# Kernel optimization log

Measured on AMD Instinct MI355X. Metric: run time of the kernel, lower is better.

The kernel has to match this reference:

```python
import jax, jax.numpy as jnp
import numpy as np

B, S, D = 2, 2048, 2048
H, HK, HD = 16, 4, 128          # query heads, kv heads, head dim (H*HD == D)
HID = 4 * D                      # SwiGLU hidden (mult=4)
WIN, SINK = 1024, 4              # sliding window, attention sink tokens
EPS = 1e-6
ROPE_BASE = 10000.0


def rmsnorm(x, g):
    return x * jax.lax.rsqrt(jnp.mean(x * x, axis=-1, keepdims=True) + EPS) * g


def rope_tables(seq_len, head_dim):
    inv = 1.0 / (ROPE_BASE ** (jnp.arange(0, head_dim, 2, dtype=jnp.float32) / head_dim))
    ang = jnp.arange(seq_len, dtype=jnp.float32)[:, None] * inv[None, :]  # [S, HD/2]
    return jnp.cos(ang), jnp.sin(ang)


def apply_rope(x, cos, sin):
    # x: [B, S, h, HD]; rotate-half convention
    x1, x2 = jnp.split(x, 2, axis=-1)
    c = cos[None, :, None, :]
    s = sin[None, :, None, :]
    return jnp.concatenate([x1 * c - x2 * s, x2 * c + x1 * s], axis=-1)


def setup_inputs() -> dict:
    key = jax.random.key(0)
    ks = jax.random.split(key, 10)
    p = 0.02
    return {
        "x": jax.random.normal(ks[0], (B, S, D), dtype=jnp.float32),
        "g1": jnp.ones((D,), dtype=jnp.float32),
        "g2": jnp.ones((D,), dtype=jnp.float32),
        "wq": jax.random.normal(ks[1], (D, H * HD), dtype=jnp.float32) * p,
        "wk": jax.random.normal(ks[2], (D, HK * HD), dtype=jnp.float32) * p,
        "wv": jax.random.normal(ks[3], (D, HK * HD), dtype=jnp.float32) * p,
        "wo": jax.random.normal(ks[4], (H * HD, D), dtype=jnp.float32) * p,
        "w_gate": jax.random.normal(ks[5], (D, HID), dtype=jnp.float32) * p,
        "w_up": jax.random.normal(ks[6], (D, HID), dtype=jnp.float32) * p,
        "w_down": jax.random.normal(ks[7], (HID, D), dtype=jnp.float32) * p,
    }


def reference(x, g1, g2, wq, wk, wv, wo, w_gate, w_up, w_down):
    # ---- pre-norm attention ----
    h = rmsnorm(x, g1)
    q = (h @ wq).reshape(B, S, H, HD)
    k = (h @ wk).reshape(B, S, HK, HD)
    v = (h @ wv).reshape(B, S, HK, HD)

    cos, sin = rope_tables(S, HD)
    q = apply_rope(q, cos, sin)
    k = apply_rope(k, cos, sin)

    # GQA: expand kv heads to query heads
    rep = H // HK
    k = jnp.repeat(k, rep, axis=2)  # [B, S, H, HD]
    v = jnp.repeat(v, rep, axis=2)

    scores = jnp.einsum("bqhd,bkhd->bhqk", q, k) / jnp.sqrt(jnp.float32(HD))

    # causal + sliding-window + attention-sink mask
    i = jnp.arange(S)[:, None]
    j = jnp.arange(S)[None, :]
    allowed = (j <= i) & (((i - j) < WIN) | (j < SINK))  # [S, S]
    scores = jnp.where(allowed[None, None], scores, jnp.float32(-1e9))

    attn = jax.nn.softmax(scores, axis=-1)
    a = jnp.einsum("bhqk,bkhd->bqhd", attn, v).reshape(B, S, H * HD) @ wo

    x = x + a

    # ---- pre-norm SwiGLU FFN ----
    h2 = rmsnorm(x, g2)
    ffn = (jax.nn.silu(h2 @ w_gate) * (h2 @ w_up)) @ w_down
    return x + ffn
```

## Files before the change

### kernel.cpp

```cpp
#include <hip/hip_runtime.h>
#include <hip/hip_bf16.h>
#include <stdint.h>

#define TOK 4096
#define SEQ 2048
#define DM 2048
#define NH 16
#define NKV 4
#define HDIM 128
#define HID 8192
#define WIN 1024
#define SINKN 4

typedef float f32x4 __attribute__((ext_vector_type(4)));
typedef __bf16 bf16x8 __attribute__((ext_vector_type(8)));
typedef unsigned short u16;
typedef unsigned int u32;

#define VM(n) asm volatile("s_waitcnt vmcnt(" #n ")" ::: "memory")
#define LG(n) asm volatile("s_waitcnt lgkmcnt(" #n ")" ::: "memory")
#define SCHED0 __builtin_amdgcn_sched_barrier(0)

__device__ __forceinline__ u16 f2bf(float f) {
  union { float f; u32 u; } v; v.f = f;
  return (u16)((v.u + 0x7fffu + ((v.u >> 16) & 1u)) >> 16);
}
__device__ __forceinline__ float bf2f(u16 h) {
  union { u32 u; float f; } v; v.u = ((u32)h) << 16;
  return v.f;
}
__device__ __forceinline__ f32x4 mfma16(bf16x8 a, bf16x8 b, f32x4 c) {
  return __builtin_amdgcn_mfma_f32_16x16x32_bf16(a, b, c, 0, 0, 0);
}
__device__ __forceinline__ void gld16(const u16* g, u16* l) {
  __builtin_amdgcn_global_load_lds(
      (const __attribute__((address_space(1))) u32*)g,
      (__attribute__((address_space(3))) u32*)l, 16, 0, 0);
}
__device__ __forceinline__ void bar() {
  asm volatile("s_barrier" ::: "memory");
}
__device__ __forceinline__ void swz_rc(int c, int& row, int& k8) {
  row = 2 * (c >> 3) + (((c >> 2) & 1) ^ ((c >> 4) & 1));
  k8 = (c & 3) ^ (row & 3);
}
__device__ __forceinline__ void raster8(int wg, int nwg, int nbx, int& bx, int& by) {
  int cpx = nwg >> 3;
  int s = (wg & 7) * cpx + (wg >> 3);
  by = 8 * (s / (8 * nbx)) + (s & 7);
  bx = (s >> 3) % nbx;
}

__global__ __launch_bounds__(256)
void wtrans(const float* __restrict__ in, u16* __restrict__ out, int K, int N)
{
  __shared__ float t[32][33];
  int tx = threadIdx.x & 31, ty = threadIdx.x >> 5;
  int bx = blockIdx.x, by = blockIdx.y;
  #pragma unroll
  for (int i = 0; i < 4; i++) {
    int r = ty + i * 8;
    t[r][tx] = in[(size_t)(by * 32 + r) * N + bx * 32 + tx];
  }
  __syncthreads();
  #pragma unroll
  for (int i = 0; i < 4; i++) {
    int r = ty + i * 8;
    out[(size_t)(bx * 32 + r) * K + by * 32 + tx] = f2bf(t[tx][r]);
  }
}

__global__ __launch_bounds__(256)
void vtrans(const u16* __restrict__ in, int ld, u16* __restrict__ out)
{
  __shared__ u16 t[32][33];
  int tx = threadIdx.x & 31, ty = threadIdx.x >> 5;
  int bx = blockIdx.x;
  int by = blockIdx.y;
  #pragma unroll
  for (int i = 0; i < 4; i++) {
    int r = ty + i * 8;
    t[r][tx] = in[(size_t)(by * 32 + r) * ld + bx * 32 + tx];
  }
  __syncthreads();
  int b = (by * 32) >> 11;
  int s0 = (by * 32) & (SEQ - 1);
  #pragma unroll
  for (int i = 0; i < 4; i++) {
    int c = bx * 32 + ty + i * 8;
    out[(size_t)(b * (NKV * HDIM) + c) * SEQ + s0 + tx] = t[tx][ty + i * 8];
  }
}

__global__ __launch_bounds__(256)
void rope_table_k(float* __restrict__ ct, float* __restrict__ st)
{
  int idx = blockIdx.x * 256 + threadIdx.x;
  int pos = idx >> 6, d = idx & 63;
  float inv = powf(10000.0f, -(float)d / 64.0f);
  float a = (float)pos * inv;
  ct[idx] = cosf(a);
  st[idx] = sinf(a);
}

__global__ void rope_apply_k(u16* __restrict__ q, int ld,
                             const float* __restrict__ ct,
                             const float* __restrict__ st, float scale)
{
  int t = blockIdx.x;
  int hh = threadIdx.x >> 6;
  int d = threadIdx.x & 63;
  int pos = t & (SEQ - 1);
  size_t base = (size_t)t * ld + hh * HDIM + d;
  float x1 = bf2f(q[base]), x2 = bf2f(q[base + 64]);
  float c = ct[pos * 64 + d], s = st[pos * 64 + d];
  q[base]      = f2bf((x1 * c - x2 * s) * scale);
  q[base + 64] = f2bf((x2 * c + x1 * s) * scale);
}

__global__ __launch_bounds__(256)
void rmsnorm_k(const float* __restrict__ x, const float* __restrict__ g,
               u16* __restrict__ o)
{
  int row = blockIdx.x;
  int tid = threadIdx.x;
  const float* xr = x + (size_t)row * DM;
  float4 v0 = *(const float4*)(xr + tid * 8);
  float4 v1 = *(const float4*)(xr + tid * 8 + 4);
  float ss = v0.x*v0.x + v0.y*v0.y + v0.z*v0.z + v0.w*v0.w
           + v1.x*v1.x + v1.y*v1.y + v1.z*v1.z + v1.w*v1.w;
  #pragma unroll
  for (int d = 1; d < 64; d <<= 1) ss += __shfl_xor(ss, d);
  __shared__ float red[4];
  if ((tid & 63) == 0) red[tid >> 6] = ss;
  __syncthreads();
  float inv = rsqrtf((red[0] + red[1] + red[2] + red[3]) * (1.0f / DM) + 1e-6f);
  float4 g0 = *(const float4*)(g + tid * 8);
  float4 g1 = *(const float4*)(g + tid * 8 + 4);
  ushort4 o0, o1;
  o0.x = f2bf(v0.x * inv * g0.x); o0.y = f2bf(v0.y * inv * g0.y);
  o0.z = f2bf(v0.z * inv * g0.z); o0.w = f2bf(v0.w * inv * g0.w);
  o1.x = f2bf(v1.x * inv * g1.x); o1.y = f2bf(v1.y * inv * g1.y);
  o1.z = f2bf(v1.z * inv * g1.z); o1.w = f2bf(v1.w * inv * g1.w);
  *(ushort4*)(o + (size_t)row * DM + tid * 8) = o0;
  *(ushort4*)(o + (size_t)row * DM + tid * 8 + 4) = o1;
}

template<int EPI>
__global__ __launch_bounds__(512, 1)
void gemmp(const u16* __restrict__ A, const u16* __restrict__ Bt,
           u16* __restrict__ Cb, float* __restrict__ Cf,
           const float* __restrict__ X, int M, int N, int K, int nbx)
{
  constexpr int ASZ = 128 * 64;
  constexpr int SLOT = ASZ + 256 * 64;
  __shared__ u16 lds[3 * SLOT];

  int bx, by;
  raster8(blockIdx.x, gridDim.x, nbx, bx, by);
  int m0 = by * 128;
  int n0 = bx * 256;

  int tid = threadIdx.x;
  int l = tid & 63, w = tid >> 6;
  int l16 = l & 15, lg = l >> 4;
  int wr = w >> 2, wc = w & 3;

  int aoff[4][2], boff[4][2];
  #pragma unroll
  for (int m = 0; m < 4; m++)
    #pragma unroll
    for (int kk = 0; kk < 2; kk++) {
      int row = wr * 64 + m * 16 + l16;
      aoff[m][kk] = ((row * 128 + kk * 64 + lg * 16) ^ ((row & 7) << 4)) >> 1;
    }
  #pragma unroll
  for (int n = 0; n < 4; n++)
    #pragma unroll
    for (int kk = 0; kk < 2; kk++) {
      int br = wc * 64 + n * 16 + l16;
      boff[n][kk] = ASZ + (((br * 128 + kk * 64 + lg * 16) ^ ((br & 7) << 4)) >> 1);
    }

  int urow = tid >> 3;
  int cc = (tid & 7) ^ (urow & 7);
  const u16* pA[2];
  const u16* pB[4];
  pA[0] = A + (size_t)(m0 + urow) * K + cc * 8;
  pA[1] = A + (size_t)(m0 + 64 + urow) * K + cc * 8;
  #pragma unroll
  for (int u = 0; u < 4; u++)
    pB[u] = Bt + (size_t)(n0 + u * 64 + urow) * K + cc * 8;

  const int NT = K >> 6;

  auto stA = [&](int tt, int u) {
    gld16(pA[u] + (size_t)tt * 64, lds + (tt % 3) * SLOT + u * 4096 + tid * 8);
  };
  auto stB = [&](int tt, int u) {
    gld16(pB[u] + (size_t)tt * 64, lds + (tt % 3) * SLOT + ASZ + u * 4096 + tid * 8);
  };

  #pragma unroll
  for (int u = 0; u < 4; u++) stB(0, u);
  stA(0, 0); stA(0, 1);
  #pragma unroll
  for (int u = 0; u < 4; u++) stB(1, u);
  stA(1, 0); stA(1, 1);
  VM(6);
  bar();

  f32x4 acc[4][4];
  f32x4 zero = {0.f, 0.f, 0.f, 0.f};
  #pragma unroll
  for (int m = 0; m < 4; m++)
    #pragma unroll
    for (int n = 0; n < 4; n++) acc[m][n] = zero;

  for (int t = 0; t < NT; ++t) {
    u16* cur = lds + (t % 3) * SLOT;
    const bool st = (t + 2 < NT);

    if (st) { stB(t + 2, 0); stB(t + 2, 1); stB(t + 2, 2); }
    bf16x8 a[4][2], b[2][2], c2[2][2];
    #pragma unroll
    for (int m = 0; m < 4; m++) {
      a[m][0] = *(const bf16x8*)(cur + aoff[m][0]);
      a[m][1] = *(const bf16x8*)(cur + aoff[m][1]);
    }
    #pragma unroll
    for (int n = 0; n < 2; n++) {
      b[n][0] = *(const bf16x8*)(cur + boff[n][0]);
      b[n][1] = *(const bf16x8*)(cur + boff[n][1]);
    }
    SCHED0;
    #pragma unroll
    for (int n = 0; n < 2; n++) {
      c2[n][0] = *(const bf16x8*)(cur + boff[n + 2][0]);
      c2[n][1] = *(const bf16x8*)(cur + boff[n + 2][1]);
    }
    bar();
    LG(4);
    SCHED0;
    __builtin_amdgcn_s_setprio(1);
    #pragma unroll
    for (int m = 0; m < 4; m++)
      #pragma unroll
      for (int n = 0; n < 2; n++) {
        acc[m][n] = mfma16(a[m][0], b[n][0], acc[m][n]);
        acc[m][n] = mfma16(a[m][1], b[n][1], acc[m][n]);
      }
    __builtin_amdgcn_s_setprio(0);
    SCHED0;
    bar();

    if (st) { stB(t + 2, 3); stA(t + 2, 0); stA(t + 2, 1); }
    if (st) { VM(6); }
    else if (t + 1 < NT) { VM(0); }
    bar();
    LG(0);
    SCHED0;
    __builtin_amdgcn_s_setprio(1);
    #pragma unroll
    for (int m = 0; m < 4; m++)
      #pragma unroll
      for (int n = 0; n < 2; n++) {
        acc[m][n + 2] = mfma16(a[m][0], c2[n][0], acc[m][n + 2]);
        acc[m][n + 2] = mfma16(a[m][1], c2[n][1], acc[m][n + 2]);
      }
    __builtin_amdgcn_s_setprio(0);
    SCHED0;
    bar();
  }

  #pragma unroll
  for (int m = 0; m < 4; m++) {
    int row = m0 + wr * 64 + m * 16 + lg * 4;
    #pragma unroll
    for (int n = 0; n < 4; n++) {
      int col = n0 + wc * 64 + n * 16 + l16;
      #pragma unroll
      for (int r = 0; r < 4; r++) {
        size_t idx = (size_t)(row + r) * N + col;
        float v = acc[m][n][r];
        if (EPI == 0) {
          Cb[idx] = f2bf(v);
        } else if (EPI == 1) {
          Cf[idx] = X[idx] + v;
        } else {
          Cf[idx] += v;
        }
      }
    }
  }
}

__global__ __launch_bounds__(512, 1)
void gemm256gu(const u16* __restrict__ A, const u16* __restrict__ Bg,
               const u16* __restrict__ Bu, u16* __restrict__ Gu,
               int K, int nbx)
{
  constexpr int SLOT = 32768;
  __shared__ u16 lds[2 * SLOT];

  int bx, by;
  raster8(blockIdx.x, gridDim.x, nbx, bx, by);
  int m0 = by * 256, n0 = bx * 128;

  int tid = threadIdx.x;
  int l = tid & 63, w = tid >> 6;
  int l16 = l & 15, lg = l >> 4;
  int wr = w >> 2, wc = w & 3;

  int sw = (l16 & 7) << 4;
  int aoffk[2], boffk[2];
  #pragma unroll
  for (int kk = 0; kk < 2; kk++) {
    aoffk[kk] = ((wr * 128 + l16) * 128 + ((kk * 64 + lg * 16) ^ sw)) >> 1;
    boffk[kk] = 16384 + ((((wc * 32 + l16) * 128) + ((kk * 64 + lg * 16) ^ sw)) >> 1);
  }

  int rh = tid >> 3;
  int cc = (tid & 7) ^ (rh & 7);
  const u16* pA0[2]; const u16* pA1[2]; const u16* pBg[2]; const u16* pBu[2];
  #pragma unroll
  for (int ll = 0; ll < 2; ll++) {
    pA0[ll] = A + (size_t)(m0 + ll * 64 + rh) * K + cc * 8;
    pA1[ll] = A + (size_t)(m0 + 128 + ll * 64 + rh) * K + cc * 8;
    pBg[ll] = Bg + (size_t)(n0 + ll * 64 + rh) * K + cc * 8;
    pBu[ll] = Bu + (size_t)(n0 + ll * 64 + rh) * K + cc * 8;
  }

  const int NT = K >> 6;

  auto stA0 = [&](int tt) {
    u16* d = lds + (tt & 1) * SLOT;
    gld16(pA0[0] + (size_t)tt * 64, d + tid * 8);
    gld16(pA0[1] + (size_t)tt * 64, d + 4096 + tid * 8);
  };
  auto stA1 = [&](int tt) {
    u16* d = lds + (tt & 1) * SLOT + 8192;
    gld16(pA1[0] + (size_t)tt * 64, d + tid * 8);
    gld16(pA1[1] + (size_t)tt * 64, d + 4096 + tid * 8);
  };
  auto stBg = [&](int tt) {
    u16* d = lds + (tt & 1) * SLOT + 16384;
    gld16(pBg[0] + (size_t)tt * 64, d + tid * 8);
    gld16(pBg[1] + (size_t)tt * 64, d + 4096 + tid * 8);
  };
  auto stBu = [&](int tt) {
    u16* d = lds + (tt & 1) * SLOT + 16384 + 8192;
    gld16(pBu[0] + (size_t)tt * 64, d + tid * 8);
    gld16(pBu[1] + (size_t)tt * 64, d + 4096 + tid * 8);
  };

  stA0(0); stA1(0); stBg(0); stBu(0);
  stA0(1); stBg(1); stBu(1);
  VM(6);
  bar();

  f32x4 acc[8][4];
  f32x4 zero = {0.f, 0.f, 0.f, 0.f};
  #pragma unroll
  for (int m = 0; m < 8; m++)
    #pragma unroll
    for (int n = 0; n < 4; n++) acc[m][n] = zero;

  for (int t = 0; t < NT; ++t) {
    u16* cur = lds + (t & 1) * SLOT;

    if (t + 1 < NT) stA1(t + 1);
    bf16x8 a0[4], a1[4], b0[4];
    #pragma unroll
    for (int m = 0; m < 4; m++)
      a0[m] = *(const bf16x8*)(cur + aoffk[0] + m * 1024);
    #pragma unroll
    for (int n = 0; n < 4; n++)
      b0[n] = *(const bf16x8*)(cur + boffk[0] + (n & 1) * 1024 + (n >> 1) * 8192);
    SCHED0;
    #pragma unroll
    for (int m = 0; m < 4; m++)
      a1[m] = *(const bf16x8*)(cur + aoffk[0] + 4096 + m * 1024);
    bar();
    LG(4);
    SCHED0;
    __builtin_amdgcn_s_setprio(1);
    #pragma unroll
    for (int m = 0; m < 4; m++)
      #pragma unroll
      for (int n = 0; n < 4; n++)
        acc[m][n] = mfma16(a0[m], b0[n], acc[m][n]);
    __builtin_amdgcn_s_setprio(0);
    SCHED0;
    bar();

    bf16x8 a2[4], b1[4];
    #pragma unroll
    for (int m = 0; m < 4; m++)
      a2[m] = *(const bf16x8*)(cur + aoffk[1] + m * 1024);
    #pragma unroll
    for (int n = 0; n < 4; n++)
      b1[n] = *(const bf16x8*)(cur + boffk[1] + (n & 1) * 1024 + (n >> 1) * 8192);
    bar();
    LG(8);
    SCHED0;
    __builtin_amdgcn_s_setprio(1);
    #pragma unroll
    for (int m = 0; m < 4; m++)
      #pragma unroll
      for (int n = 0; n < 4; n++)
        acc[4 + m][n] = mfma16(a1[m], b0[n], acc[4 + m][n]);
    __builtin_amdgcn_s_setprio(0);
    SCHED0;
    bar();

    bf16x8 a3[4];
    #pragma unroll
    for (int m = 0; m < 4; m++)
      a3[m] = *(const bf16x8*)(cur + aoffk[1] + 4096 + m * 1024);
    bar();
    LG(4);
    SCHED0;
    __builtin_amdgcn_s_setprio(1);
    #pragma unroll
    for (int m = 0; m < 4; m++)
      #pragma unroll
      for (int n = 0; n < 4; n++)
        acc[m][n] = mfma16(a2[m], b1[n], acc[m][n]);
    __builtin_amdgcn_s_setprio(0);
    SCHED0;
    bar();

    if (t + 2 < NT) { stA0(t + 2); stBg(t + 2); stBu(t + 2); }
    bar();
    LG(0);
    SCHED0;
    __builtin_amdgcn_s_setprio(1);
    #pragma unroll
    for (int m = 0; m < 4; m++)
      #pragma unroll
      for (int n = 0; n < 4; n++)
        acc[4 + m][n] = mfma16(a3[m], b1[n], acc[4 + m][n]);
    __builtin_amdgcn_s_setprio(0);
    SCHED0;
    if (t + 2 < NT) { VM(6); }
    else if (t + 1 < NT) { VM(0); }
    bar();
  }

  #pragma unroll
  for (int m = 0; m < 8; m++) {
    int row = m0 + wr * 128 + m * 16 + lg * 4;
    #pragma unroll
    for (int n = 0; n < 2; n++) {
      int col = n0 + wc * 32 + n * 16 + l16;
      #pragma unroll
      for (int r = 0; r < 4; r++) {
        float gt = acc[m][n][r];
        float up = acc[m][n + 2][r];
        float sg = gt / (1.0f + __expf(-gt));
        Gu[(size_t)(row + r) * HID + col] = f2bf(sg * up);
      }
    }
  }
}

__global__ __launch_bounds__(256)
void attn_k(const u16* __restrict__ qb, int ldq,
            const u16* __restrict__ kb, int ldk,
            const u16* __restrict__ vbt, u16* __restrict__ ao)
{
  int q0 = blockIdx.x * 128;
  int h = blockIdx.y;
  int b = blockIdx.z;
  int hk = h >> 2;
  int tid = threadIdx.x;
  int w = tid >> 6, l = tid & 63;
  int l16 = l & 15, lg = l >> 4;

  __shared__ u16 Ks[32 * 128];
  __shared__ u16 Vt[128 * 32];
  __shared__ u16 Ps[4][32 * 40];
  u16* Pw = Ps[w];

  bf16x8 qf[2][4];
  #pragma unroll
  for (int m = 0; m < 2; m++)
    #pragma unroll
    for (int kd = 0; kd < 4; kd++) {
      int row = q0 + w * 32 + m * 16 + l16;
      qf[m][kd] = *(const bf16x8*)(qb + (size_t)(b * SEQ + row) * ldq
                                   + h * HDIM + kd * 32 + lg * 8);
    }

  f32x4 oacc[2][8];
  float mrun[2][4], lrun[2][4];
  f32x4 zero = {0.f, 0.f, 0.f, 0.f};
  #pragma unroll
  for (int m = 0; m < 2; m++) {
    #pragma unroll
    for (int nd = 0; nd < 8; nd++) oacc[m][nd] = zero;
    #pragma unroll
    for (int r = 0; r < 4; r++) { mrun[m][r] = -1e9f; lrun[m][r] = 0.f; }
  }

  int kr0 = tid >> 4,        kc0 = (tid & 15) ^ (kr0 & 7);
  int kr1 = (tid + 256) >> 4, kc1 = (tid & 15) ^ (kr1 & 7);
  int vd0, vk0, vd1, vk1;
  swz_rc(tid, vd0, vk0);
  swz_rc(tid + 256, vd1, vk1);
  const u16* kbase = kb + (size_t)(b * SEQ) * ldk + hk * HDIM;
  const u16* vbase = vbt + (size_t)(b * NKV + hk) * HDIM * SEQ;

  int koff[2][4];
  #pragma unroll
  for (int n = 0; n < 2; n++)
    #pragma unroll
    for (int kd = 0; kd < 4; kd++) {
      int key = n * 16 + l16;
      koff[n][kd] = ((key * 128) + kd * 32 + lg * 8) ^ ((key & 7) * 8);
    }
  int voff[8];
  #pragma unroll
  for (int nd = 0; nd < 8; nd++) {
    int d = nd * 16 + l16;
    voff[nd] = (d * 32 + lg * 8) ^ ((d & 7) * 8);
  }

  int lo = (q0 >= WIN) ? ((q0 - (WIN - 1)) >> 5) : 0;
  int hi = (q0 + 127) >> 5;

  for (int it = (lo > 0 ? lo - 1 : 0); it <= hi; ++it) {
    int kt = (it < lo) ? 0 : it;
    gld16(kbase + (size_t)(kt * 32 + kr0) * ldk + kc0 * 8, Ks + tid * 8);
    gld16(kbase + (size_t)(kt * 32 + kr1) * ldk + kc1 * 8, Ks + (tid + 256) * 8);
    gld16(vbase + (size_t)vd0 * SEQ + kt * 32 + vk0 * 8, Vt + tid * 8);
    gld16(vbase + (size_t)vd1 * SEQ + kt * 32 + vk1 * 8, Vt + (tid + 256) * 8);
    __syncthreads();

    f32x4 sacc[2][2];
    sacc[0][0] = zero; sacc[0][1] = zero; sacc[1][0] = zero; sacc[1][1] = zero;
    #pragma unroll
    for (int kd = 0; kd < 4; kd++) {
      bf16x8 kf0 = *(const bf16x8*)(Ks + koff[0][kd]);
      bf16x8 kf1 = *(const bf16x8*)(Ks + koff[1][kd]);
      #pragma unroll
      for (int m = 0; m < 2; m++) {
        sacc[m][0] = mfma16(qf[m][kd], kf0, sacc[m][0]);
        sacc[m][1] = mfma16(qf[m][kd], kf1, sacc[m][1]);
      }
    }

    #pragma unroll
    for (int m = 0; m < 2; m++) {
      float sc[4];
      #pragma unroll
      for (int r = 0; r < 4; r++) {
        int i = q0 + w * 32 + m * 16 + lg * 4 + r;
        int j0 = kt * 32 + l16;
        int j1 = j0 + 16;
        float s0 = sacc[m][0][r];
        float s1 = sacc[m][1][r];
        bool ok0 = (j0 <= i) && ((i - j0 < WIN) || (j0 < SINKN));
        bool ok1 = (j1 <= i) && ((i - j1 < WIN) || (j1 < SINKN));
        s0 = ok0 ? s0 : -1e9f;
        s1 = ok1 ? s1 : -1e9f;
        float mx = fmaxf(s0, s1);
        mx = fmaxf(mx, __shfl_xor(mx, 1));
        mx = fmaxf(mx, __shfl_xor(mx, 2));
        mx = fmaxf(mx, __shfl_xor(mx, 4));
        mx = fmaxf(mx, __shfl_xor(mx, 8));
        float mold = mrun[m][r];
        float mnew = fmaxf(mold, mx);
        float scl = __expf(mold - mnew);
        mrun[m][r] = mnew;
        float p0 = __expf(s0 - mnew);
        float p1 = __expf(s1 - mnew);
        int prow = m * 16 + lg * 4 + r;
        Pw[prow * 40 + l16] = f2bf(p0);
        Pw[prow * 40 + 16 + l16] = f2bf(p1);
        float ps = p0 + p1;
        ps += __shfl_xor(ps, 1);
        ps += __shfl_xor(ps, 2);
        ps += __shfl_xor(ps, 4);
        ps += __shfl_xor(ps, 8);
        lrun[m][r] = lrun[m][r] * scl + ps;
        sc[r] = scl;
      }
      #pragma unroll
      for (int nd = 0; nd < 8; nd++) {
        oacc[m][nd][0] *= sc[0];
        oacc[m][nd][1] *= sc[1];
        oacc[m][nd][2] *= sc[2];
        oacc[m][nd][3] *= sc[3];
      }
    }

    bf16x8 pa0 = *(const bf16x8*)(Pw + l16 * 40 + lg * 8);
    bf16x8 pa1 = *(const bf16x8*)(Pw + (16 + l16) * 40 + lg * 8);
    #pragma unroll
    for (int nd = 0; nd < 8; nd++) {
      bf16x8 vf = *(const bf16x8*)(Vt + voff[nd]);
      oacc[0][nd] = mfma16(pa0, vf, oacc[0][nd]);
      oacc[1][nd] = mfma16(pa1, vf, oacc[1][nd]);
    }
    __syncthreads();
  }

  #pragma unroll
  for (int m = 0; m < 2; m++)
    #pragma unroll
    for (int r = 0; r < 4; r++) {
      float invl = 1.0f / lrun[m][r];
      int row = q0 + w * 32 + m * 16 + lg * 4 + r;
      #pragma unroll
      for (int nd = 0; nd < 8; nd++) {
        int col = nd * 16 + l16;
        ao[(size_t)(b * SEQ + row) * (NH * HDIM) + h * HDIM + col] =
            f2bf(oacc[m][nd][r] * invl);
      }
    }
}

extern "C" void kernel_launch(void* const* d_in, const int* in_sizes, int n_in,
                              void* d_out, int out_size, void* d_ws, size_t ws_size,
                              hipStream_t stream)
{
  (void)in_sizes; (void)n_in; (void)out_size;
  const float* x  = (const float*)d_in[0];
  const float* g1 = (const float*)d_in[1];
  const float* g2 = (const float*)d_in[2];
  const float* wq = (const float*)d_in[3];
  const float* wk = (const float*)d_in[4];
  const float* wv = (const float*)d_in[5];
  const float* wo = (const float*)d_in[6];
  const float* wg = (const float*)d_in[7];
  const float* wu = (const float*)d_in[8];
  const float* wd = (const float*)d_in[9];
  float* out = (float*)d_out;

  char* ws = (char*)d_ws;
  size_t off = 0;
  auto alloc = [&](size_t bytes) {
    char* p = ws + off;
    off += (bytes + 255) & ~(size_t)255;
    return p;
  };
  const int NQKV = 3072;
  u16* wqkv_t = (u16*)alloc((size_t)NQKV * DM * 2);
  u16* wo_t   = (u16*)alloc((size_t)DM * DM * 2);
  u16* wg_t   = (u16*)alloc((size_t)HID * DM * 2);
  u16* wu_t   = (u16*)alloc((size_t)HID * DM * 2);
  u16* wd_t   = (u16*)alloc((size_t)DM * HID * 2);
  u16* hb     = (u16*)alloc((size_t)TOK * DM * 2);
  char* span0 = ws + off;
  u16* qkvb   = (u16*)alloc((size_t)TOK * NQKV * 2);
  u16* vbt    = (u16*)alloc((size_t)TOK * NKV * HDIM * 2);
  u16* aob    = (u16*)alloc((size_t)TOK * NH * HDIM * 2);
  size_t span_used = (size_t)(ws + off - span0);
  size_t gu_need = (size_t)TOK * HID * 2;
  if (gu_need > span_used) alloc(gu_need - span_used);
  u16* gu = (u16*)span0;
  float* ct  = (float*)alloc((size_t)SEQ * 64 * 4);
  float* st  = (float*)alloc((size_t)SEQ * 64 * 4);
  if (off > ws_size) return;

  dim3 blk(256);
  dim3 blk512(512);

  wtrans<<<dim3(DM / 32, DM / 32), blk, 0, stream>>>(wq, wqkv_t, DM, DM);
  wtrans<<<dim3((NKV * HDIM) / 32, DM / 32), blk, 0, stream>>>(wk, wqkv_t + (size_t)DM * DM, DM, NKV * HDIM);
  wtrans<<<dim3((NKV * HDIM) / 32, DM / 32), blk, 0, stream>>>(wv, wqkv_t + (size_t)(DM + NKV * HDIM) * DM, DM, NKV * HDIM);
  wtrans<<<dim3(DM / 32, DM / 32), blk, 0, stream>>>(wo, wo_t, DM, DM);
  wtrans<<<dim3(HID / 32, DM / 32), blk, 0, stream>>>(wg, wg_t, DM, HID);
  wtrans<<<dim3(HID / 32, DM / 32), blk, 0, stream>>>(wu, wu_t, DM, HID);
  wtrans<<<dim3(DM / 32, HID / 32), blk, 0, stream>>>(wd, wd_t, HID, DM);

  rope_table_k<<<SEQ * 64 / 256, blk, 0, stream>>>(ct, st);
  rmsnorm_k<<<TOK, blk, 0, stream>>>(x, g1, hb);

  gemmp<0><<<dim3((NQKV / 256) * (TOK / 128)), blk512, 0, stream>>>(
      hb, wqkv_t, qkvb, nullptr, nullptr, TOK, NQKV, DM, NQKV / 256);

  rope_apply_k<<<TOK, dim3(NH * 64), 0, stream>>>(qkvb, NQKV, ct, st, 0.08838834764831845f);
  rope_apply_k<<<TOK, dim3(NKV * 64), 0, stream>>>(qkvb + DM, NQKV, ct, st, 1.0f);
  vtrans<<<dim3((NKV * HDIM) / 32, TOK / 32), blk, 0, stream>>>(qkvb + DM + NKV * HDIM, NQKV, vbt);

  attn_k<<<dim3(SEQ / 128, NH, 2), blk, 0, stream>>>(qkvb, NQKV, qkvb + DM, NQKV, vbt, aob);

  gemmp<1><<<dim3((DM / 256) * (TOK / 128)), blk512, 0, stream>>>(
      aob, wo_t, nullptr, out, x, TOK, DM, DM, DM / 256);
  rmsnorm_k<<<TOK, blk, 0, stream>>>(out, g2, hb);

  gemm256gu<<<dim3((HID / 128) * (TOK / 256)), blk512, 0, stream>>>(
      hb, wg_t, wu_t, gu, DM, HID / 128);

  gemmp<3><<<dim3((DM / 256) * (TOK / 128)), blk512, 0, stream>>>(
      gu, wd_t, nullptr, out, nullptr, TOK, DM, HID, DM / 256);
}
```

Baseline: 796.4 us.

## Generalize 256x256 GEMM kernel, add register prefetch pipeline and split-K down projection

Turns the gate/up-specific 256-row GEMM into a templated kernel that also handles plain 256x256 tiles and split-K with atomic accumulation. The loop is restructured so the next tile's first A/B fragments are loaded from LDS during the last MFMA phase, hiding LDS read latency. The QKV projection moves to 256x256 tiles for more reuse per block. The down projection is split across two K halves with atomicAdd into the residual output to get more blocks running, which adds atomic traffic and makes the float summation order nondeterministic.

```diff
diff --git a/kernel.cpp b/kernel.cpp
--- a/kernel.cpp
+++ b/kernel.cpp
@@ -295,17 +295,24 @@
   }
 }
 
+template<int EPI, int GU, int SPLITK>
 __global__ __launch_bounds__(512, 1)
-void gemm256gu(const u16* __restrict__ A, const u16* __restrict__ Bg,
-               const u16* __restrict__ Bu, u16* __restrict__ Gu,
-               int K, int nbx)
+void gemm256(const u16* __restrict__ A, const u16* __restrict__ B1,
+             const u16* __restrict__ B2, u16* __restrict__ Cb,
+             float* __restrict__ Cf, int Kst, int NT, int N, int nbx)
 {
   constexpr int SLOT = 32768;
   __shared__ u16 lds[2 * SLOT];
 
+  int wg = blockIdx.x;
+  int nwg = gridDim.x;
+  int kh = 0;
+  if (SPLITK) { int half = nwg >> 1; kh = (wg >= half); wg -= kh * half; nwg = half; }
   int bx, by;
-  raster8(blockIdx.x, gridDim.x, nbx, bx, by);
-  int m0 = by * 256, n0 = bx * 128;
+  raster8(wg, nwg, nbx, bx, by);
+  int m0 = by * 256;
+  int n0 = bx * (GU ? 128 : 256);
+  size_t k0 = (size_t)kh * NT * 64;
 
   int tid = threadIdx.x;
   int l = tid & 63, w = tid >> 6;
@@ -317,21 +324,24 @@
   #pragma unroll
   for (int kk = 0; kk < 2; kk++) {
     aoffk[kk] = ((wr * 128 + l16) * 128 + ((kk * 64 + lg * 16) ^ sw)) >> 1;
-    boffk[kk] = 16384 + ((((wc * 32 + l16) * 128) + ((kk * 64 + lg * 16) ^ sw)) >> 1);
+    int bbase = GU ? (wc * 32 + l16) : (wc * 64 + l16);
+    boffk[kk] = 16384 + (((bbase * 128) + ((kk * 64 + lg * 16) ^ sw)) >> 1);
   }
 
   int rh = tid >> 3;
   int cc = (tid & 7) ^ (rh & 7);
-  const u16* pA0[2]; const u16* pA1[2]; const u16* pBg[2]; const u16* pBu[2];
+  const u16* pA0[2]; const u16* pA1[2]; const u16* pB[4];
   #pragma unroll
   for (int ll = 0; ll < 2; ll++) {
-    pA0[ll] = A + (size_t)(m0 + ll * 64 + rh) * K + cc * 8;
-    pA1[ll] = A + (size_t)(m0 + 128 + ll * 64 + rh) * K + cc * 8;
-    pBg[ll] = Bg + (size_t)(n0 + ll * 64 + rh) * K + cc * 8;
-    pBu[ll] = Bu + (size_t)(n0 + ll * 64 + rh) * K + cc * 8;
-  }
-
-  const int NT = K >> 6;
+    pA0[ll] = A + (size_t)(m0 + ll * 64 + rh) * Kst + k0 + cc * 8;
+    pA1[ll] = A + (size_t)(m0 + 128 + ll * 64 + rh) * Kst + k0 + cc * 8;
+  }
+  #pragma unroll
+  for (int u = 0; u < 4; u++) {
+    if (GU) pB[u] = (u < 2 ? B1 + (size_t)(n0 + u * 64 + rh) * Kst
+                           : B2 + (size_t)(n0 + (u - 2) * 64 + rh) * Kst) + k0 + cc * 8;
+    else    pB[u] = B1 + (size_t)(n0 + u * 64 + rh) * Kst + k0 + cc * 8;
+  }
 
   auto stA0 = [&](int tt) {
     u16* d = lds + (tt & 1) * SLOT;
@@ -343,19 +353,15 @@
     gld16(pA1[0] + (size_t)tt * 64, d + tid * 8);
     gld16(pA1[1] + (size_t)tt * 64, d + 4096 + tid * 8);
   };
-  auto stBg = [&](int tt) {
+  auto stB4 = [&](int tt) {
     u16* d = lds + (tt & 1) * SLOT + 16384;
-    gld16(pBg[0] + (size_t)tt * 64, d + tid * 8);
-    gld16(pBg[1] + (size_t)tt * 64, d + 4096 + tid * 8);
+    #pragma unroll
+    for (int u = 0; u < 4; u++)
+      gld16(pB[u] + (size_t)tt * 64, d + u * 4096 + tid * 8);
   };
-  auto stBu = [&](int tt) {
-    u16* d = lds + (tt & 1) * SLOT + 16384 + 8192;
-    gld16(pBu[0] + (size_t)tt * 64, d + tid * 8);
-    gld16(pBu[1] + (size_t)tt * 64, d + 4096 + tid * 8);
-  };
-
-  stA0(0); stA1(0); stBg(0); stBu(0);
-  stA0(1); stBg(1); stBu(1);
+
+  stA0(0); stA1(0); stB4(0);
+  stA0(1); stB4(1);
   VM(6);
   bar();
 
@@ -366,100 +372,128 @@
     #pragma unroll
     for (int n = 0; n < 4; n++) acc[m][n] = zero;
 
+  bf16x8 aA[4], aB[4], aC[4], aD[4], bb0[4], bb1[4];
+  {
+    u16* s0 = lds;
+    #pragma unroll
+    for (int m = 0; m < 4; m++) aA[m] = *(const bf16x8*)(s0 + aoffk[0] + m * 1024);
+    #pragma unroll
+    for (int n = 0; n < 4; n++)
+      bb0[n] = *(const bf16x8*)(s0 + boffk[0] + (GU ? ((n & 1) * 1024 + (n >> 1) * 8192)
+                                                    : (n * 1024)));
+  }
+
   for (int t = 0; t < NT; ++t) {
     u16* cur = lds + (t & 1) * SLOT;
-
+    u16* nxt = lds + ((t + 1) & 1) * SLOT;
+
+    #pragma unroll
+    for (int m = 0; m < 4; m++) aB[m] = *(const bf16x8*)(cur + aoffk[0] + 4096 + m * 1024);
     if (t + 1 < NT) stA1(t + 1);
-    bf16x8 a0[4], a1[4], b0[4];
+    bar();
+    LG(4);
+    SCHED0;
+    __builtin_amdgcn_s_setprio(1);
     #pragma unroll
     for (int m = 0; m < 4; m++)
-      a0[m] = *(const bf16x8*)(cur + aoffk[0] + m * 1024);
+      #pragma unroll
+      for (int n = 0; n < 4; n++)
+        acc[m][n] = mfma16(aA[m], bb0[n], acc[m][n]);
+    __builtin_amdgcn_s_setprio(0);
+    SCHED0;
+    bar();
+
+    #pragma unroll
+    for (int m = 0; m < 4; m++) aC[m] = *(const bf16x8*)(cur + aoffk[1] + m * 1024);
     #pragma unroll
     for (int n = 0; n < 4; n++)
-      b0[n] = *(const bf16x8*)(cur + boffk[0] + (n & 1) * 1024 + (n >> 1) * 8192);
-    SCHED0;
+      bb1[n] = *(const bf16x8*)(cur + boffk[1] + (GU ? ((n & 1) * 1024 + (n >> 1) * 8192)
+                                                     : (n * 1024)));
+    bar();
+    LG(8);
+    SCHED0;
+    __builtin_amdgcn_s_setprio(1);
     #pragma unroll
     for (int m = 0; m < 4; m++)
-      a1[m] = *(const bf16x8*)(cur + aoffk[0] + 4096 + m * 1024);
-    bar();
-    LG(4);
+      #pragma unroll
+      for (int n = 0; n < 4; n++)
+        acc[4 + m][n] = mfma16(aB[m], bb0[n], acc[4 + m][n]);
+    __builtin_amdgcn_s_setprio(0);
+    SCHED0;
+    bar();
+
+    #pragma unroll
+    for (int m = 0; m < 4; m++) aD[m] = *(const bf16x8*)(cur + aoffk[1] + 4096 + m * 1024);
+    bar();
+    LG(0);
     SCHED0;
     __builtin_amdgcn_s_setprio(1);
     #pragma unroll
     for (int m = 0; m < 4; m++)
       #pragma unroll
       for (int n = 0; n < 4; n++)
-        acc[m][n] = mfma16(a0[m], b0[n], acc[m][n]);
+        acc[m][n] = mfma16(aC[m], bb1[n], acc[m][n]);
     __builtin_amdgcn_s_setprio(0);
     SCHED0;
     bar();
 
-    bf16x8 a2[4], b1[4];
+    if (t + 2 < NT) {
+      stA0(t + 2); stB4(t + 2);
+      VM(6);
+    } else if (t + 1 < NT) {
+      VM(0);
+    }
+    bar();
+    if (t + 1 < NT) {
+      #pragma unroll
+      for (int m = 0; m < 4; m++) aA[m] = *(const bf16x8*)(nxt + aoffk[0] + m * 1024);
+      #pragma unroll
+      for (int n = 0; n < 4; n++)
+        bb0[n] = *(const bf16x8*)(nxt + boffk[0] + (GU ? ((n & 1) * 1024 + (n >> 1) * 8192)
+                                                       : (n * 1024)));
+    }
+    LG(8);
+    SCHED0;
+    __builtin_amdgcn_s_setprio(1);
     #pragma unroll
     for (int m = 0; m < 4; m++)
-      a2[m] = *(const bf16x8*)(cur + aoffk[1] + m * 1024);
-    #pragma unroll
-    for (int n = 0; n < 4; n++)
-      b1[n] = *(const bf16x8*)(cur + boffk[1] + (n & 1) * 1024 + (n >> 1) * 8192);
-    bar();
-    LG(8);
-    SCHED0;
-    __builtin_amdgcn_s_setprio(1);
-    #pragma unroll
-    for (int m = 0; m < 4; m++)
       #pragma unroll
       for (int n = 0; n < 4; n++)
-        acc[4 + m][n] = mfma16(a1[m], b0[n], acc[4 + m][n]);
+        acc[4 + m][n] = mfma16(aD[m], bb1[n], acc[4 + m][n]);
     __builtin_amdgcn_s_setprio(0);
     SCHED0;
     bar();
-
-    bf16x8 a3[4];
-    #pragma unroll
-    for (int m = 0; m < 4; m++)
-      a3[m] = *(const bf16x8*)(cur + aoffk[1] + 4096 + m * 1024);
-    bar();
-    LG(4);
-    SCHED0;
-    __builtin_amdgcn_s_setprio(1);
-    #pragma unroll
-    for (int m = 0; m < 4; m++)
-      #pragma unroll
-      for (int n = 0; n < 4; n++)
-        acc[m][n] = mfma16(a2[m], b1[n], acc[m][n]);
-    __builtin_amdgcn_s_setprio(0);
-    SCHED0;
-    bar();
-
-    if (t + 2 < NT) { stA0(t + 2); stBg(t + 2); stBu(t + 2); }
-    bar();
-    LG(0);
-    SCHED0;
-    __builtin_amdgcn_s_setprio(1);
-    #pragma unroll
-    for (int m = 0; m < 4; m++)
-      #pragma unroll
-      for (int n = 0; n < 4; n++)
-        acc[4 + m][n] = mfma16(a3[m], b1[n], acc[4 + m][n]);
-    __builtin_amdgcn_s_setprio(0);
-    SCHED0;
-    if (t + 2 < NT) { VM(6); }
-    else if (t + 1 < NT) { VM(0); }
-    bar();
-  }
-
-  #pragma unroll
-  for (int m = 0; m < 8; m++) {
-    int row = m0 + wr * 128 + m * 16 + lg * 4;
-    #pragma unroll
-    for (int n = 0; n < 2; n++) {
-      int col = n0 + wc * 32 + n * 16 + l16;
-      #pragma unroll
-      for (int r = 0; r < 4; r++) {
-        float gt = acc[m][n][r];
-        float up = acc[m][n + 2][r];
-        float sg = gt / (1.0f + __expf(-gt));
-        Gu[(size_t)(row + r) * HID + col] = f2bf(sg * up);
+  }
+
+  if (GU) {
+    #pragma unroll
+    for (int m = 0; m < 8; m++) {
+      int row = m0 + wr * 128 + m * 16 + lg * 4;
+      #pragma unroll
+      for (int n = 0; n < 2; n++) {
+        int col = n0 + wc * 32 + n * 16 + l16;
+        #pragma unroll
+        for (int r = 0; r < 4; r++) {
+          float gt = acc[m][n][r];
+          float up = acc[m][n + 2][r];
+          float sg = gt / (1.0f + __expf(-gt));
+          Cb[(size_t)(row + r) * N + col] = f2bf(sg * up);
+        }
+      }
+    }
+  } else {
+    #pragma unroll
+    for (int m = 0; m < 8; m++) {
+      int row = m0 + wr * 128 + m * 16 + lg * 4;
+      #pragma unroll
+      for (int n = 0; n < 4; n++) {
+        int col = n0 + wc * 64 + n * 16 + l16;
+        #pragma unroll
+        for (int r = 0; r < 4; r++) {
+          size_t idx = (size_t)(row + r) * N + col;
+          if (EPI == 0) Cb[idx] = f2bf(acc[m][n][r]);
+          else          atomicAdd(Cf + idx, acc[m][n][r]);
+        }
       }
     }
   }
@@ -679,8 +713,8 @@
   rope_table_k<<<SEQ * 64 / 256, blk, 0, stream>>>(ct, st);
   rmsnorm_k<<<TOK, blk, 0, stream>>>(x, g1, hb);
 
-  gemmp<0><<<dim3((NQKV / 256) * (TOK / 128)), blk512, 0, stream>>>(
-      hb, wqkv_t, qkvb, nullptr, nullptr, TOK, NQKV, DM, NQKV / 256);
+  gemm256<0, 0, 0><<<dim3((NQKV / 256) * (TOK / 256)), blk512, 0, stream>>>(
+      hb, wqkv_t, nullptr, qkvb, nullptr, DM, DM / 64, NQKV, NQKV / 256);
 
   rope_apply_k<<<TOK, dim3(NH * 64), 0, stream>>>(qkvb, NQKV, ct, st, 0.08838834764831845f);
   rope_apply_k<<<TOK, dim3(NKV * 64), 0, stream>>>(qkvb + DM, NQKV, ct, st, 1.0f);
@@ -692,9 +726,9 @@
       aob, wo_t, nullptr, out, x, TOK, DM, DM, DM / 256);
   rmsnorm_k<<<TOK, blk, 0, stream>>>(out, g2, hb);
 
-  gemm256gu<<<dim3((HID / 128) * (TOK / 256)), blk512, 0, stream>>>(
-      hb, wg_t, wu_t, gu, DM, HID / 128);
-
-  gemmp<3><<<dim3((DM / 256) * (TOK / 128)), blk512, 0, stream>>>(
-      gu, wd_t, nullptr, out, nullptr, TOK, DM, HID, DM / 256);
-}
+  gemm256<0, 1, 0><<<dim3((HID / 128) * (TOK / 256)), blk512, 0, stream>>>(
+      hb, wg_t, wu_t, gu, nullptr, DM, DM / 64, HID, HID / 128);
+
+  gemm256<4, 0, 1><<<dim3(2 * (DM / 256) * (TOK / 256)), blk512, 0, stream>>>(
+      gu, wd_t, nullptr, nullptr, out, HID, HID / 128, DM, DM / 256);
+}
```

After: 781.8 us. No clear change (-1.8%).
